# Kernel optimization log

Measured on AMD Instinct MI355X. Metric: run time of the kernel, lower is better.

The kernel has to match this reference:

```python
import jax, jax.numpy as jnp
import numpy as np

TAU = 2.0   # spikingjelly LIFNode default tau
VTH = 1.0   # config.vthreshold

@jax.custom_vjp
def atan_spike(x):
    # heaviside forward, ATan surrogate backward (spikingjelly surrogate.ATan, alpha=2)
    return (x >= 0).astype(x.dtype)

def _atan_fwd(x):
    return atan_spike(x), x

def _atan_bwd(x, g):
    alpha = 2.0
    return (g * (alpha / 2.0) / (1.0 + (jnp.pi / 2.0 * alpha * x) ** 2),)

atan_spike.defvjp(_atan_fwd, _atan_bwd)

def layer_norm(x, eps=1e-6):
    m = jnp.mean(x, axis=-1, keepdims=True)
    v = jnp.mean((x - m) ** 2, axis=-1, keepdims=True)
    return (x - m) * jax.lax.rsqrt(v + eps)

def time_shift(x):
    # ZeroPad2d((0,0,1,-1)): xx[:, t] = x[:, t-1], xx[:, 0] = 0
    return jnp.pad(x, ((0, 0), (1, 0), (0, 0)))[:, :-1]

def lif_multistep(x4):
    # spikingjelly LIFNode, step_mode='m', decay_input=True, hard reset to v_reset=0
    def step(v, xt):
        v = v + (xt - v) / TAU
        s = atan_spike(v - VTH)
        return v * (1.0 - s), s
    _, spikes = jax.lax.scan(step, jnp.zeros_like(x4[0]), x4)
    return spikes

def wkv(w, u, k, v):
    # RWKV-v4 numerically-stable WKV scan. w: [C] (negative), u: [C], k,v: [B,T,C]
    B, T, C = k.shape
    def step(carry, kv):
        aa, bb, pp = carry
        kt, vt = kv
        ww = u + kt
        p = jnp.maximum(pp, ww)
        e1 = jnp.exp(pp - p); e2 = jnp.exp(ww - p)
        y = (e1 * aa + e2 * vt) / (e1 * bb + e2)
        ww2 = pp + w
        p2 = jnp.maximum(ww2, kt)
        f1 = jnp.exp(ww2 - p2); f2 = jnp.exp(kt - p2)
        return (f1 * aa + f2 * vt, f1 * bb + f2, p2), y
    init = (jnp.zeros((B, C), k.dtype), jnp.zeros((B, C), k.dtype),
            jnp.full((B, C), -1e38, k.dtype))
    _, ys = jax.lax.scan(step, init, (jnp.moveaxis(k, 1, 0), jnp.moveaxis(v, 1, 0)))
    return jnp.moveaxis(ys, 0, 1)

def time_mix(h, time_decay, time_first, tmk, tmv, tmr, Wk, Wv, Wr, Wo):
    xx = time_shift(h)
    xk = h * tmk + xx * (1 - tmk)
    xv = h * tmv + xx * (1 - tmv)
    xr = h * tmr + xx * (1 - tmr)
    k = jnp.einsum('btc,oc->bto', xk, Wk)
    v = jnp.einsum('btc,oc->bto', xv, Wv)
    sr = jax.nn.sigmoid(jnp.einsum('btc,oc->bto', xr, Wr))
    y = wkv(-jnp.exp(time_decay), time_first, k, v)
    return jnp.einsum('btc,oc->bto', sr * y, Wo)

def channel_mix(h, cmk, cmr, Wck, Wcv, Wcr):
    xx = time_shift(h)
    xk = h * cmk + xx * (1 - cmk)
    xr = h * cmr + xx * (1 - cmr)
    k = jnp.square(jax.nn.relu(jnp.einsum('btc,hc->bth', xk, Wck)))
    kv = jnp.einsum('bth,ch->btc', k, Wcv)
    return jax.nn.sigmoid(jnp.einsum('btc,oc->bto', xr, Wcr)) * kv

def _forward(x, rt, time_decay, time_first, tmix_k, tmix_v, tmix_r,
             Wk, Wv, Wr, Wo, cmix_k, cmix_r, Wck, Wcv, Wcr,
             Wrm, brm, Wam, bam):
    B, P1, C = x.shape
    xc = jnp.concatenate([x, jnp.broadcast_to(rt, (B, P1, C))], axis=1)  # [B, 2*P1, C]
    att = time_mix(layer_norm(xc), time_decay, time_first,
                   tmix_k, tmix_v, tmix_r, Wk, Wv, Wr, Wo)
    att = lif_multistep(jnp.broadcast_to(att, (4,) + att.shape)).mean(0)
    xc = xc + att
    ffn = channel_mix(layer_norm(xc), cmix_k, cmix_r, Wck, Wcv, Wcr)
    ffn = lif_multistep(jnp.broadcast_to(ffn, (4,) + ffn.shape)).mean(0)
    xc = xc + ffn
    xo, rtok = xc[:, :P1], xc[:, P1:]
    r = jnp.einsum('bpc,qc->bpq', rtok, Wrm) + brm   # restruction_token_MLP [B,P1,P1]
    r = jnp.swapaxes(r, 1, 2)                        # permute(0,2,1)
    r = jnp.einsum('bpq,cq->bpc', r, Wam) + bam      # another_MLP [B,P1,C]
    return xo + xo * r

def setup_inputs() -> dict:
    key = jax.random.key(0)
    ks = jax.random.split(key, 20)
    B, P1, C = 8, 256, 1024
    H = 4 * C
    s = 0.02
    f32 = jnp.float32
    return {
        'x': jax.random.normal(ks[0], (B, P1, C), f32),
        'rt': jax.random.normal(ks[1], (1, P1, C), f32) * 0.5,
        'time_decay': jax.random.normal(ks[2], (C,), f32),
        'time_first': jax.random.normal(ks[3], (C,), f32) * 0.3,
        'tmix_k': jax.random.uniform(ks[4], (1, 1, C), f32),
        'tmix_v': jax.random.uniform(ks[5], (1, 1, C), f32),
        'tmix_r': jax.random.uniform(ks[6], (1, 1, C), f32),
        'Wk': jax.random.normal(ks[7], (C, C), f32) * s,
        'Wv': jax.random.normal(ks[8], (C, C), f32) * s,
        'Wr': jax.random.normal(ks[9], (C, C), f32) * s,
        'Wo': jax.random.normal(ks[10], (C, C), f32) * s,
        'cmix_k': jax.random.uniform(ks[11], (1, 1, C), f32),
        'cmix_r': jax.random.uniform(ks[12], (1, 1, C), f32),
        'Wck': jax.random.normal(ks[13], (H, C), f32) * s,
        'Wcv': jax.random.normal(ks[14], (C, H), f32) * s,
        'Wcr': jax.random.normal(ks[15], (C, C), f32) * s,
        'Wrm': jax.random.normal(ks[16], (P1, C), f32) * s,
        'brm': jax.random.normal(ks[17], (P1,), f32) * s,
        'Wam': jax.random.normal(ks[18], (C, P1), f32) * s,
        'bam': jax.random.normal(ks[19], (C,), f32) * s,
    }

def reference(x, rt, time_decay, time_first, tmix_k, tmix_v, tmix_r,
              Wk, Wv, Wr, Wo, cmix_k, cmix_r, Wck, Wcv, Wcr,
              Wrm, brm, Wam, bam):
    return _forward(x, rt, time_decay, time_first, tmix_k, tmix_v, tmix_r,
                    Wk, Wv, Wr, Wo, cmix_k, cmix_r, Wck, Wcv, Wcr,
                    Wrm, brm, Wam, bam)
```

## Files before the change

kernel.cpp:

```cpp
#include <hip/hip_runtime.h>
#include <hip/hip_bf16.h>
#include <math.h>
#include <stdint.h>

#define TB_ 8
#define TT_ 512
#define TC_ 1024
#define WKV_NCH 32
#define WKV_L 16

typedef __attribute__((ext_vector_type(8))) short bf16x8;
typedef __attribute__((ext_vector_type(4))) short s16x4;
typedef __attribute__((ext_vector_type(4))) float f32x4;

__device__ __forceinline__ float b2f(short u) {
  union { unsigned int i; float f; } x;
  x.i = ((unsigned int)(unsigned short)u) << 16;
  return x.f;
}
__device__ __forceinline__ short f2b(float f) {
  __hip_bfloat16 h = __float2bfloat16(f);
  return __builtin_bit_cast(short, h);
}
__device__ __forceinline__ float sigm(float x) { return 1.0f / (1.0f + expf(-x)); }

__device__ __forceinline__ float lif4(float a) {
  float v = 0.0f, acc = 0.0f;
#pragma unroll
  for (int i = 0; i < 4; ++i) {
    v += (a - v) * 0.5f;
    float s = (v >= 1.0f) ? 1.0f : 0.0f;
    acc += s;
    v *= (1.0f - s);
  }
  return acc * 0.25f;
}

__device__ __forceinline__ void gload16(const void* g, void* l) {
  __builtin_amdgcn_global_load_lds(
      (__attribute__((address_space(1))) void*)(g),
      (__attribute__((address_space(3))) void*)(l), 16, 0, 0);
}

template <int N>
__device__ __forceinline__ void waitv() {
  if constexpr (N == 0)  asm volatile("s_waitcnt vmcnt(0)" ::: "memory");
  else if constexpr (N == 2)  asm volatile("s_waitcnt vmcnt(2)" ::: "memory");
  else if constexpr (N == 4)  asm volatile("s_waitcnt vmcnt(4)" ::: "memory");
  else if constexpr (N == 8)  asm volatile("s_waitcnt vmcnt(8)" ::: "memory");
  else if constexpr (N == 12) asm volatile("s_waitcnt vmcnt(12)" ::: "memory");
  else static_assert(N == 0, "unsupported vmcnt");
}
__device__ __forceinline__ void barrier_() {
  asm volatile("s_barrier" ::: "memory");
}


__global__ __launch_bounds__(256) void ln_mix3(
    const float* __restrict__ x, const float* __restrict__ rt,
    const float* __restrict__ tmk, const float* __restrict__ tmv,
    const float* __restrict__ tmr, float* __restrict__ xc,
    short* __restrict__ xk, short* __restrict__ xv, short* __restrict__ xr) {
  __shared__ float red[256];
  int row = blockIdx.x;
  int t = row & 511, b = row >> 9;
  int tid = threadIdx.x;
  const float* src = (t < 256) ? x + (int64_t)(b * 256 + t) * TC_
                               : rt + (int64_t)(t - 256) * TC_;
  float4 v = ((const float4*)src)[tid];
  ((float4*)(xc + (int64_t)row * TC_))[tid] = v;
  red[tid] = v.x + v.y + v.z + v.w;
  __syncthreads();
  for (int off = 128; off > 0; off >>= 1) {
    if (tid < off) red[tid] += red[tid + off];
    __syncthreads();
  }
  float mean = red[0] * (1.0f / 1024.0f);
  __syncthreads();
  float dx = v.x - mean, dy = v.y - mean, dz = v.z - mean, dw = v.w - mean;
  red[tid] = dx * dx + dy * dy + dz * dz + dw * dw;
  __syncthreads();
  for (int off = 128; off > 0; off >>= 1) {
    if (tid < off) red[tid] += red[tid + off];
    __syncthreads();
  }
  float rs = 1.0f / sqrtf(red[0] * (1.0f / 1024.0f) + 1e-6f);
  float c0 = dx * rs, c1 = dy * rs, c2 = dz * rs, c3 = dw * rs;
  float p0 = 0.f, p1 = 0.f, p2 = 0.f, p3 = 0.f;
  if (t > 0) {
    int tp = t - 1;
    const float* srcp = (tp < 256) ? x + (int64_t)(b * 256 + tp) * TC_
                                   : rt + (int64_t)(tp - 256) * TC_;
    __syncthreads();
    float4 w4 = ((const float4*)srcp)[tid];
    red[tid] = w4.x + w4.y + w4.z + w4.w;
    __syncthreads();
    for (int off = 128; off > 0; off >>= 1) {
      if (tid < off) red[tid] += red[tid + off];
      __syncthreads();
    }
    float meanp = red[0] * (1.0f / 1024.0f);
    __syncthreads();
    float ex = w4.x - meanp, ey = w4.y - meanp, ez = w4.z - meanp,
          ew = w4.w - meanp;
    red[tid] = ex * ex + ey * ey + ez * ez + ew * ew;
    __syncthreads();
    for (int off = 128; off > 0; off >>= 1) {
      if (tid < off) red[tid] += red[tid + off];
      __syncthreads();
    }
    float rsp = 1.0f / sqrtf(red[0] * (1.0f / 1024.0f) + 1e-6f);
    p0 = ex * rsp; p1 = ey * rsp; p2 = ez * rsp; p3 = ew * rsp;
  }
  int c = tid * 4;
  int64_t o = (int64_t)row * TC_ + c;
  float m0, m1, m2, m3;
  s16x4 ov;
  m0 = tmk[c]; m1 = tmk[c + 1]; m2 = tmk[c + 2]; m3 = tmk[c + 3];
  ov.x = f2b(c0 * m0 + p0 * (1.0f - m0));
  ov.y = f2b(c1 * m1 + p1 * (1.0f - m1));
  ov.z = f2b(c2 * m2 + p2 * (1.0f - m2));
  ov.w = f2b(c3 * m3 + p3 * (1.0f - m3));
  *(s16x4*)(xk + o) = ov;
  m0 = tmv[c]; m1 = tmv[c + 1]; m2 = tmv[c + 2]; m3 = tmv[c + 3];
  ov.x = f2b(c0 * m0 + p0 * (1.0f - m0));
  ov.y = f2b(c1 * m1 + p1 * (1.0f - m1));
  ov.z = f2b(c2 * m2 + p2 * (1.0f - m2));
  ov.w = f2b(c3 * m3 + p3 * (1.0f - m3));
  *(s16x4*)(xv + o) = ov;
  m0 = tmr[c]; m1 = tmr[c + 1]; m2 = tmr[c + 2]; m3 = tmr[c + 3];
  ov.x = f2b(c0 * m0 + p0 * (1.0f - m0));
  ov.y = f2b(c1 * m1 + p1 * (1.0f - m1));
  ov.z = f2b(c2 * m2 + p2 * (1.0f - m2));
  ov.w = f2b(c3 * m3 + p3 * (1.0f - m3));
  *(s16x4*)(xr + o) = ov;
}

__global__ __launch_bounds__(256) void ln_mix2(const float* __restrict__ xc,
                                               const float* __restrict__ cmk,
                                               const float* __restrict__ cmr,
                                               short* __restrict__ xk,
                                               short* __restrict__ xr) {
  __shared__ float red[256];
  int row = blockIdx.x;
  int t = row & 511;
  int tid = threadIdx.x;
  float4 v = ((const float4*)(xc + (int64_t)row * TC_))[tid];
  red[tid] = v.x + v.y + v.z + v.w;
  __syncthreads();
  for (int off = 128; off > 0; off >>= 1) {
    if (tid < off) red[tid] += red[tid + off];
    __syncthreads();
  }
  float mean = red[0] * (1.0f / 1024.0f);
  __syncthreads();
  float dx = v.x - mean, dy = v.y - mean, dz = v.z - mean, dw = v.w - mean;
  red[tid] = dx * dx + dy * dy + dz * dz + dw * dw;
  __syncthreads();
  for (int off = 128; off > 0; off >>= 1) {
    if (tid < off) red[tid] += red[tid + off];
    __syncthreads();
  }
  float rs = 1.0f / sqrtf(red[0] * (1.0f / 1024.0f) + 1e-6f);
  float c0 = dx * rs, c1 = dy * rs, c2 = dz * rs, c3 = dw * rs;
  float p0 = 0.f, p1 = 0.f, p2 = 0.f, p3 = 0.f;
  if (t > 0) {
    __syncthreads();
    float4 w4 = ((const float4*)(xc + (int64_t)(row - 1) * TC_))[tid];
    red[tid] = w4.x + w4.y + w4.z + w4.w;
    __syncthreads();
    for (int off = 128; off > 0; off >>= 1) {
      if (tid < off) red[tid] += red[tid + off];
      __syncthreads();
    }
    float meanp = red[0] * (1.0f / 1024.0f);
    __syncthreads();
    float ex = w4.x - meanp, ey = w4.y - meanp, ez = w4.z - meanp,
          ew = w4.w - meanp;
    red[tid] = ex * ex + ey * ey + ez * ez + ew * ew;
    __syncthreads();
    for (int off = 128; off > 0; off >>= 1) {
      if (tid < off) red[tid] += red[tid + off];
      __syncthreads();
    }
    float rsp = 1.0f / sqrtf(red[0] * (1.0f / 1024.0f) + 1e-6f);
    p0 = ex * rsp; p1 = ey * rsp; p2 = ez * rsp; p3 = ew * rsp;
  }
  int c = tid * 4;
  float k0 = cmk[c], k1 = cmk[c + 1], k2 = cmk[c + 2], k3 = cmk[c + 3];
  float r0 = cmr[c], r1 = cmr[c + 1], r2 = cmr[c + 2], r3 = cmr[c + 3];
  s16x4 ok, orr;
  ok.x = f2b(c0 * k0 + p0 * (1.0f - k0));
  ok.y = f2b(c1 * k1 + p1 * (1.0f - k1));
  ok.z = f2b(c2 * k2 + p2 * (1.0f - k2));
  ok.w = f2b(c3 * k3 + p3 * (1.0f - k3));
  orr.x = f2b(c0 * r0 + p0 * (1.0f - r0));
  orr.y = f2b(c1 * r1 + p1 * (1.0f - r1));
  orr.z = f2b(c2 * r2 + p2 * (1.0f - r2));
  orr.w = f2b(c3 * r3 + p3 * (1.0f - r3));
  *(s16x4*)(xk + (int64_t)row * TC_ + c) = ok;
  *(s16x4*)(xr + (int64_t)row * TC_ + c) = orr;
}

__global__ __launch_bounds__(256) void cvt_b(const float* __restrict__ src,
                                             short* __restrict__ dst) {
  int64_t i = (int64_t)(blockIdx.x * 256 + threadIdx.x) * 8;
  float4 a = *(const float4*)(src + i);
  float4 b = *(const float4*)(src + i + 4);
  bf16x8 o;
  o[0] = f2b(a.x); o[1] = f2b(a.y); o[2] = f2b(a.z); o[3] = f2b(a.w);
  o[4] = f2b(b.x); o[5] = f2b(b.y); o[6] = f2b(b.z); o[7] = f2b(b.w);
  *(bf16x8*)(dst + i) = o;
}

__global__ __launch_bounds__(256) void cvt_rtok(const float* __restrict__ xc,
                                                short* __restrict__ dst) {
  int i = blockIdx.x * 256 + threadIdx.x;
  int b = i >> 15;
  int rem = i & 32767;
  const float* s = xc + (int64_t)b * 524288 + 262144 + (int64_t)rem * 8;
  float4 a = *(const float4*)s;
  float4 c = *(const float4*)(s + 4);
  bf16x8 o;
  o[0] = f2b(a.x); o[1] = f2b(a.y); o[2] = f2b(a.z); o[3] = f2b(a.w);
  o[4] = f2b(c.x); o[5] = f2b(c.y); o[6] = f2b(c.z); o[7] = f2b(c.w);
  *(bf16x8*)(dst + (int64_t)i * 8) = o;
}

__global__ __launch_bounds__(256) void cvt_all(
    const float* __restrict__ Wk, const float* __restrict__ Wv,
    const float* __restrict__ Wr, const float* __restrict__ Wo,
    const float* __restrict__ Wcr, const float* __restrict__ Wcv,
    const float* __restrict__ Wrm, const float* __restrict__ Wam,
    short* __restrict__ bWk, short* __restrict__ bWv, short* __restrict__ bWr,
    short* __restrict__ bWo, short* __restrict__ bWcr, short* __restrict__ bWcv,
    short* __restrict__ bWrm, short* __restrict__ bWam,
    float* __restrict__ S) {
  int bid = blockIdx.x;
  if (bid >= 4864) {
    int row = (bid - 4864) * 4 + (threadIdx.x >> 6);
    int lane = threadIdx.x & 63;
    float4 v = ((const float4*)(Wam + (int64_t)row * 256))[lane];
    float s = v.x + v.y + v.z + v.w;
    for (int off = 32; off > 0; off >>= 1) s += __shfl_down(s, off);
    if (lane == 0) S[row] = s;
    return;
  }
  const float* src; short* dst; int base;
  if (bid < 512)       { src = Wk;  dst = bWk;  base = bid; }
  else if (bid < 1024) { src = Wv;  dst = bWv;  base = bid - 512; }
  else if (bid < 1536) { src = Wr;  dst = bWr;  base = bid - 1024; }
  else if (bid < 2048) { src = Wo;  dst = bWo;  base = bid - 1536; }
  else if (bid < 2560) { src = Wcr; dst = bWcr; base = bid - 2048; }
  else if (bid < 4608) { src = Wcv; dst = bWcv; base = bid - 2560; }
  else if (bid < 4736) { src = Wrm; dst = bWrm; base = bid - 4608; }
  else                 { src = Wam; dst = bWam; base = bid - 4736; }
  int64_t i = ((int64_t)base * 256 + threadIdx.x) * 8;
  float4 a = *(const float4*)(src + i);
  float4 b = *(const float4*)(src + i + 4);
  bf16x8 o;
  o[0] = f2b(a.x); o[1] = f2b(a.y); o[2] = f2b(a.z); o[3] = f2b(a.w);
  o[4] = f2b(b.x); o[5] = f2b(b.y); o[6] = f2b(b.z); o[7] = f2b(b.w);
  *(bf16x8*)(dst + i) = o;
}

__global__ __launch_bounds__(256) void wkv_p1(const float* __restrict__ td,
                                              const short* __restrict__ K,
                                              const short* __restrict__ V,
                                              float* __restrict__ Ca,
                                              float* __restrict__ Da,
                                              float* __restrict__ Qa) {
  int bx = blockIdx.x;
  int ch = bx >> 5;
  int b = (bx >> 2) & 7;
  int c = (bx & 3) * 256 + threadIdx.x;
  float w = -expf(td[c]);
  float aa = 0.0f, bb = 0.0f, pp = -1e38f;
  int64_t base = ((int64_t)b * TT_ + ch * WKV_L) * TC_ + c;
#pragma unroll
  for (int t = 0; t < WKV_L; ++t) {
    int64_t o = base + (int64_t)t * TC_;
    float kt = b2f(K[o]), vt = b2f(V[o]);
    float ww2 = pp + w;
    float p2 = fmaxf(ww2, kt);
    float e1 = expf(ww2 - p2);
    float e2 = expf(kt - p2);
    aa = e1 * aa + e2 * vt;
    bb = e1 * bb + e2;
    pp = p2;
  }
  int idx = ch * 8192 + b * 1024 + c;
  Ca[idx] = aa; Da[idx] = bb; Qa[idx] = pp;
}

__global__ __launch_bounds__(256) void wkv_p2(const float* __restrict__ td,
                                              const float* __restrict__ Ca,
                                              const float* __restrict__ Da,
                                              const float* __restrict__ Qa,
                                              float* __restrict__ Aa,
                                              float* __restrict__ Ba,
                                              float* __restrict__ Pa) {
  int i = blockIdx.x * 256 + threadIdx.x;
  int c = i & (TC_ - 1);
  float wL = -expf(td[c]) * (float)WKV_L;
  float aa = 0.0f, bb = 0.0f, pp = -1e38f;
#pragma unroll 4
  for (int ch = 0; ch < WKV_NCH; ++ch) {
    int idx = ch * 8192 + i;
    Aa[idx] = aa; Ba[idx] = bb; Pa[idx] = pp;
    float ppw = pp + wL;
    float q = Qa[idx];
    float p2 = fmaxf(ppw, q);
    float ea = expf(ppw - p2);
    float eb = expf(q - p2);
    aa = aa * ea + Ca[idx] * eb;
    bb = bb * ea + Da[idx] * eb;
    pp = p2;
  }
}

__global__ __launch_bounds__(256) void wkv_p3(const float* __restrict__ td,
                                              const float* __restrict__ tf,
                                              const short* __restrict__ K,
                                              const short* __restrict__ V,
                                              const short* __restrict__ SR,
                                              short* __restrict__ SRY,
                                              const float* __restrict__ Aa,
                                              const float* __restrict__ Ba,
                                              const float* __restrict__ Pa) {
  int bx = blockIdx.x;
  int ch = bx >> 5;
  int b = (bx >> 2) & 7;
  int c = (bx & 3) * 256 + threadIdx.x;
  float w = -expf(td[c]);
  float u = tf[c];
  int idx = ch * 8192 + b * 1024 + c;
  float aa = Aa[idx], bb = Ba[idx], pp = Pa[idx];
  int64_t base = ((int64_t)b * TT_ + ch * WKV_L) * TC_ + c;
#pragma unroll
  for (int t = 0; t < WKV_L; ++t) {
    int64_t o = base + (int64_t)t * TC_;
    float kt = b2f(K[o]), vt = b2f(V[o]);
    float ww = u + kt;
    float p = fmaxf(pp, ww);
    float E1 = expf(pp - p);
    float E2 = expf(ww - p);
    float y = (E1 * aa + E2 * vt) / (E1 * bb + E2);
    SRY[o] = f2b(y * b2f(SR[o]));
    float ww2 = pp + w;
    float p2 = fmaxf(ww2, kt);
    float e1 = expf(ww2 - p2);
    float e2 = expf(kt - p2);
    aa = e1 * aa + e2 * vt;
    bb = e1 * bb + e2;
    pp = p2;
  }
}

template <int EPI>
__global__ __launch_bounds__(512, 1) void gemm4p(
    const short* __restrict__ A, const short* __restrict__ B,
    void* __restrict__ Cp, int M, int N, int K, int Kst,
    const float* __restrict__ e0, const float* __restrict__ e1,
    const float* __restrict__ e2, const void* __restrict__ e3) {
  __shared__ short lds[2 * 32768];
  const int tid = threadIdx.x;

  const unsigned gx = gridDim.x, gy = gridDim.y;
  const unsigned nwg = gx * gy;
  const unsigned lin = blockIdx.x + gx * blockIdx.y;
  const unsigned cs = nwg >> 3;
  const unsigned nl = (lin & 7) * cs + (lin >> 3);
  const unsigned bxs = nl % gx;
  const unsigned bys = nl / gx;

  const int brow = bys * 128;
  const int bcol = bxs * 128;

  const int srow = ((tid >> 6) << 4) + (tid & 15);
  const int skc = ((tid >> 4) & 3) * 8;
  const short* gA = A + (int64_t)(brow + srow) * Kst + skc;
  const short* gB = B + (int64_t)(bcol + srow) * Kst + skc;

  const int lane = tid & 63, wid = tid >> 6;
  const int wr = wid >> 2, wc = wid & 3;

  f32x4 acc[4][2] = {};

#define RD_A(rb, kh, m) \
  (*(const bf16x8*)(lds + (rb) * 32768 + (kh) * 8192 + (wr * 4 + (m)) * 512 + lane * 8))
#define RD_B(rb, kh, n) \
  (*(const bf16x8*)(lds + (rb) * 32768 + 16384 + (kh) * 8192 + (wc * 2 + (n)) * 512 + lane * 8))
#define ST_A(sb, kh, kt) \
  gload16(gA + (kt) * 64 + (kh) * 32, lds + (sb) * 32768 + (kh) * 8192 + tid * 8)
#define ST_B(sb, kh, kt) \
  gload16(gB + (kt) * 64 + (kh) * 32, lds + (sb) * 32768 + 16384 + (kh) * 8192 + tid * 8)
#define MM(am, bn, i, j) \
  acc[i][j] = __builtin_amdgcn_mfma_f32_16x16x32_bf16(am, bn, acc[i][j], 0, 0, 0)

  const int nt = K / 64;
  ST_A(0, 0, 0); ST_B(0, 0, 0); ST_A(0, 1, 0); ST_B(0, 1, 0);
  waitv<2>();
  barrier_();

  for (int t = 0; t < nt - 1; ++t) {
    const int rb = t & 1, sb = rb ^ 1, kn = t + 1;
    {
      bf16x8 a0 = RD_A(rb, 0, 0), a1 = RD_A(rb, 0, 1);
      bf16x8 b0 = RD_B(rb, 0, 0), b1 = RD_B(rb, 0, 1);
      ST_A(sb, 0, kn);
      MM(a0, b0, 0, 0); MM(a0, b1, 0, 1); MM(a1, b0, 1, 0); MM(a1, b1, 1, 1);
      barrier_();
      bf16x8 a2 = RD_A(rb, 0, 2), a3 = RD_A(rb, 0, 3);
      ST_B(sb, 0, kn);
      MM(a2, b0, 2, 0); MM(a2, b1, 2, 1); MM(a3, b0, 3, 0); MM(a3, b1, 3, 1);
      waitv<2>();
      barrier_();
    }
    {
      bf16x8 a0 = RD_A(rb, 1, 0), a1 = RD_A(rb, 1, 1);
      bf16x8 b0 = RD_B(rb, 1, 0), b1 = RD_B(rb, 1, 1);
      ST_A(sb, 1, kn);
      MM(a0, b0, 0, 0); MM(a0, b1, 0, 1); MM(a1, b0, 1, 0); MM(a1, b1, 1, 1);
      barrier_();
      bf16x8 a2 = RD_A(rb, 1, 2), a3 = RD_A(rb, 1, 3);
      ST_B(sb, 1, kn);
      MM(a2, b0, 2, 0); MM(a2, b1, 2, 1); MM(a3, b0, 3, 0); MM(a3, b1, 3, 1);
      waitv<2>();
      barrier_();
    }
  }
  {
    waitv<0>();
    barrier_();
    const int rb = (nt - 1) & 1;
#pragma unroll
    for (int kh = 0; kh < 2; ++kh) {
      bf16x8 a0 = RD_A(rb, kh, 0), a1 = RD_A(rb, kh, 1);
      bf16x8 a2 = RD_A(rb, kh, 2), a3 = RD_A(rb, kh, 3);
      bf16x8 b0 = RD_B(rb, kh, 0), b1 = RD_B(rb, kh, 1);
      MM(a0, b0, 0, 0); MM(a0, b1, 0, 1); MM(a1, b0, 1, 0); MM(a1, b1, 1, 1);
      MM(a2, b0, 2, 0); MM(a2, b1, 2, 1); MM(a3, b0, 3, 0); MM(a3, b1, 3, 1);
    }
  }
#undef RD_A
#undef RD_B
#undef ST_A
#undef ST_B
#undef MM

  const int r0 = brow + wr * 64 + (lane >> 4) * 4;
  const int c0 = bcol + wc * 32 + (lane & 15);
#pragma unroll
  for (int m = 0; m < 4; ++m) {
#pragma unroll
    for (int j = 0; j < 4; ++j) {
      int row = r0 + m * 16 + j;
#pragma unroll
      for (int n = 0; n < 2; ++n) {
        int col = c0 + n * 16;
        float v = acc[m][n][j];
        int64_t idx = (int64_t)row * N + col;
        if (EPI == 1) {
          ((short*)Cp)[idx] = f2b(sigm(v));
        } else if (EPI == 4) {
          float* XC = (float*)Cp;
          XC[idx] = XC[idx] + lif4(v);
        } else if (EPI == 5) {
          float* XC = (float*)Cp;
          float srr = b2f(((const short*)e3)[idx]);
          XC[idx] = XC[idx] + lif4(v * srr);
        }
      }
    }
  }
}

template <int BM, int BN, int EPI, int D, int MINW>
__global__ __launch_bounds__(256, MINW) void gemm_bf16(
    const short* __restrict__ A, const short* __restrict__ B,
    void* __restrict__ Cp, int M, int N, int K, int Kst,
    int64_t sA, int64_t sB, int64_t sC,
    const float* __restrict__ e0, const float* __restrict__ e1,
    const float* __restrict__ e2, const void* __restrict__ e3, int64_t sE) {
  constexpr int MF = BM / 32;
  constexpr int NF = BN / 32;
  constexpr int ASLOT = BM / 64;
  constexpr int BSLOT = BN / 64;
  constexpr int NL = ASLOT + BSLOT;
  constexpr int SBUF = (BM + BN) * 32;
  __shared__ short lds[D * SBUF];
  const int tid = threadIdx.x;

  const unsigned gx = gridDim.x, gy = gridDim.y;
  const unsigned nwg = gx * gy * gridDim.z;
  const unsigned lin = blockIdx.x + gx * (blockIdx.y + gy * blockIdx.z);
  const unsigned cs = nwg >> 3;
  const unsigned nl = (lin & 7) * cs + (lin >> 3);
  const unsigned bxs = nl % gx;
  const unsigned tmp = nl / gx;
  const unsigned bys = tmp % gy;
  const unsigned bz = tmp / gy;

  const int brow = bys * BM;
  const int bcol = bxs * BN;
  const short* Ab = A + bz * sA;
  const short* Bb = B + bz * sB;

  const int srow = ((tid >> 6) << 4) + (tid & 15);
  const int skc = ((tid >> 4) & 3) * 8;
  const short* gA[ASLOT];
  const short* gB[BSLOT];
#pragma unroll
  for (int s = 0; s < ASLOT; ++s)
    gA[s] = Ab + (int64_t)(brow + s * 64 + srow) * Kst + skc;
#pragma unroll
  for (int s = 0; s < BSLOT; ++s)
    gB[s] = Bb + (int64_t)(bcol + s * 64 + srow) * Kst + skc;

  const int lane = tid & 63, wid = tid >> 6;
  const int wr = wid >> 1, wc = wid & 1;

  f32x4 acc[MF][NF] = {};

  auto stage = [&](int buf, int k0) {
    short* d = lds + buf * SBUF;
#pragma unroll
    for (int s = 0; s < ASLOT; ++s)
      gload16(gA[s] + k0, d + s * 2048 + tid * 8);
#pragma unroll
    for (int s = 0; s < BSLOT; ++s)
      gload16(gB[s] + k0, d + BM * 32 + s * 2048 + tid * 8);
  };
  auto compute = [&](int buf) {
    const short* base = lds + buf * SBUF;
    bf16x8 af[MF], bfv[NF];
#pragma unroll
    for (int m = 0; m < MF; ++m)
      af[m] = *(const bf16x8*)(base + (wr * MF + m) * 512 + lane * 8);
#pragma unroll
    for (int n = 0; n < NF; ++n)
      bfv[n] = *(const bf16x8*)(base + BM * 32 + (wc * NF + n) * 512 + lane * 8);
#pragma unroll
    for (int m = 0; m < MF; ++m)
#pragma unroll
      for (int n = 0; n < NF; ++n)
        acc[m][n] = __builtin_amdgcn_mfma_f32_16x16x32_bf16(af[m], bfv[n],
                                                            acc[m][n], 0, 0, 0);
  };

  const int nst = K / 32;
#pragma unroll
  for (int d = 0; d < D - 1; ++d) stage(d, d * 32);
  for (int t = 0; t <= nst - D; ++t) {
    stage((t + D - 1) & (D - 1), (t + D - 1) * 32);
    waitv<(D - 1) * NL>();
    barrier_();
    compute(t & (D - 1));
    barrier_();
  }
  {
    int t = nst - D + 1;
    if constexpr (D >= 4) {
      waitv<2 * NL>(); barrier_(); compute(t & (D - 1)); barrier_(); ++t;
      waitv<1 * NL>(); barrier_(); compute(t & (D - 1)); barrier_(); ++t;
    }
    waitv<0>(); barrier_(); compute(t & (D - 1));
  }

  const int r0 = brow + wr * (BM / 2) + (lane >> 4) * 4;
  const int c0 = bcol + wc * (BN / 2) + (lane & 15);
#pragma unroll
  for (int m = 0; m < MF; ++m) {
#pragma unroll
    for (int j = 0; j < 4; ++j) {
      int row = r0 + m * 16 + j;
#pragma unroll
      for (int n = 0; n < NF; ++n) {
        int col = c0 + n * 16;
        float v = acc[m][n][j];
        int64_t idx = (int64_t)row * N + col;
        if (EPI == 0) {
          ((short*)Cp)[bz * sC + idx] = f2b(v);
        } else if (EPI == 2) {
          v = fmaxf(v, 0.0f);
          ((short*)Cp)[bz * sC + idx] = f2b(v * v);
        } else if (EPI == 3) {
          float r2 = v + e0[row] * e1[col] + e2[col];
          float xo = ((const float*)e3)[bz * sE + idx];
          ((float*)Cp)[bz * sC + idx] = xo * (1.0f + r2);
        } else if (EPI == 6) {
          ((short*)Cp)[bz * sC + idx] = f2b(bz == 2 ? sigm(v) : v);
        }
      }
    }
  }
}

extern "C" void kernel_launch(void* const* d_in, const int* in_sizes, int n_in,
                              void* d_out, int out_size, void* d_ws,
                              size_t ws_size, hipStream_t stream) {
  const float* x   = (const float*)d_in[0];
  const float* rt  = (const float*)d_in[1];
  const float* td  = (const float*)d_in[2];
  const float* tf  = (const float*)d_in[3];
  const float* tmk = (const float*)d_in[4];
  const float* tmv = (const float*)d_in[5];
  const float* tmr = (const float*)d_in[6];
  const float* Wk  = (const float*)d_in[7];
  const float* Wv  = (const float*)d_in[8];
  const float* Wr  = (const float*)d_in[9];
  const float* Wo  = (const float*)d_in[10];
  const float* cmk = (const float*)d_in[11];
  const float* cmr = (const float*)d_in[12];
  const float* Wck = (const float*)d_in[13];
  const float* Wcv = (const float*)d_in[14];
  const float* Wcr = (const float*)d_in[15];
  const float* Wrm = (const float*)d_in[16];
  const float* brm = (const float*)d_in[17];
  const float* Wam = (const float*)d_in[18];
  const float* bam = (const float*)d_in[19];
  float* out = (float*)d_out;

  const size_t MB = 1ull << 20;
  uint8_t* W8 = (uint8_t*)d_ws;
  float* XC   = (float*)(W8);
  short* S1   = (short*)(W8 + 24 * MB);
  short* S2   = (short*)(W8 + 32 * MB);
  short* S3   = (short*)(W8 + 40 * MB);
  short* bWcv = (short*)(W8 + 48 * MB);
  short* bWk  = (short*)(W8 + 56 * MB);
  short* bWo  = (short*)(W8 + 62 * MB);
  short* bWcr = (short*)(W8 + 64 * MB);
  short* bWrm = (short*)(W8 + 66 * MB);
  short* bWam = (short*)(W8 + 66 * MB + 512 * 1024);
  short* KK   = (short*)(W8 + 67 * MB);
  short* VV   = (short*)(W8 + 75 * MB);
  short* RR   = (short*)(W8 + 83 * MB);
  float* Ca   = (float*)(W8 + 91 * MB);
  float* Da   = (float*)(W8 + 92 * MB);
  float* Qa   = (float*)(W8 + 93 * MB);
  float* Aa   = (float*)(W8 + 94 * MB);
  float* Ba   = (float*)(W8 + 95 * MB);
  float* Pa   = (float*)(W8 + 96 * MB);
  short* SRY  = S1;
  short* xk2  = S2;
  short* xr2  = S3;
  short* SRR  = S1;
  short* bWck = S3;
  short* H16  = KK;
  short* rtok = S2;
  short* Mt   = (short*)(W8 + 36 * MB);
  float* Sb   = (float*)(W8 + 99 * MB);

  dim3 blk(256);
  dim3 blk512(512);

  cvt_all<<<5120, blk, 0, stream>>>(Wk, Wv, Wr, Wo, Wcr, Wcv, Wrm, Wam,
                                    bWk, bWk + 1048576, bWk + 2097152, bWo,
                                    bWcr, bWcv, bWrm, bWam, Sb);

  ln_mix3<<<TB_ * TT_, blk, 0, stream>>>(x, rt, tmk, tmv, tmr, XC, S1, S2, S3);

  gemm_bf16<128, 128, 6, 2, 3><<<dim3(8, 32, 3), blk, 0, stream>>>(
      S1, bWk, KK, 4096, 1024, 1024, 1024, 4194304, 1048576, 4194304,
      nullptr, nullptr, nullptr, nullptr, 0);
  wkv_p1<<<WKV_NCH * TB_ * 4, blk, 0, stream>>>(td, KK, VV, Ca, Da, Qa);
  wkv_p2<<<32, blk, 0, stream>>>(td, Ca, Da, Qa, Aa, Ba, Pa);
  wkv_p3<<<WKV_NCH * TB_ * 4, blk, 0, stream>>>(td, tf, KK, VV, RR, SRY,
                                                Aa, Ba, Pa);
  gemm4p<4><<<dim3(8, 32), blk512, 0, stream>>>(
      SRY, bWo, XC, 4096, 1024, 1024, 1024, nullptr, nullptr, nullptr,
      nullptr);
  ln_mix2<<<TB_ * TT_, blk, 0, stream>>>(XC, cmk, cmr, xk2, xr2);
  gemm4p<1><<<dim3(8, 32), blk512, 0, stream>>>(
      xr2, bWcr, SRR, 4096, 1024, 1024, 1024, nullptr, nullptr, nullptr,
      nullptr);
  cvt_b<<<2048, blk, 0, stream>>>(Wck, bWck);
  gemm_bf16<128, 128, 2, 2, 4><<<dim3(32, 32, 1), blk, 0, stream>>>(
      xk2, bWck, H16, 4096, 4096, 1024, 1024, 0, 0, 0,
      nullptr, nullptr, nullptr, nullptr, 0);
  gemm4p<5><<<dim3(8, 32), blk512, 0, stream>>>(
      H16, bWcv, XC, 4096, 1024, 4096, 4096, nullptr, nullptr, nullptr, SRR);
  cvt_rtok<<<1024, blk, 0, stream>>>(XC, rtok);
  gemm_bf16<64, 64, 0, 2, 2><<<dim3(4, 4, 8), blk, 0, stream>>>(
      bWrm, rtok, Mt, 256, 256, 1024, 1024, 0, (int64_t)256 * 1024,
      (int64_t)256 * 256, nullptr, nullptr, nullptr, nullptr, 0);
  gemm_bf16<64, 64, 3, 2, 2><<<dim3(16, 4, 8), blk, 0, stream>>>(
      Mt, bWam, out, 256, 1024, 256, 256, (int64_t)256 * 256, 0,
      (int64_t)256 * 1024, brm, Sb, bam, XC, (int64_t)512 * 1024);
}
```

Before: 328.6 us.

## Add 256x256-tile 512-thread GEMM with interleaved loads for channel-mix key projection

Adds a new gemm256 kernel that uses 256x256 output tiles, 8 waves, and double-buffered LDS, with global-to-LDS loads for the next k-tile interleaved between MFMA groups. It replaces the 128x128 gemm_bf16 call for the 4096x4096x1024 squared-ReLU key projection in channel mix. The larger tile raises arithmetic intensity and cuts global traffic, at the cost of one workgroup per CU (256 workgroups) and heavy register pressure from 32 accumulators per thread.

```diff
diff --git a/kernel.cpp b/kernel.cpp
--- a/kernel.cpp
+++ b/kernel.cpp
@@ -476,6 +476,160 @@
   }
 }
 
+template <int EPI>
+__global__ __launch_bounds__(512, 1) void gemm256(
+    const short* __restrict__ A, const short* __restrict__ B,
+    void* __restrict__ Cp, int M, int N, int K, int Kst) {
+  __shared__ short lds[2 * 32768];
+  const int tid = threadIdx.x;
+
+  const unsigned gx = gridDim.x, gy = gridDim.y;
+  const unsigned nwg = gx * gy;
+  const unsigned lin = blockIdx.x + gx * blockIdx.y;
+  const unsigned cs = nwg >> 3;
+  const unsigned nl = (lin & 7) * cs + (lin >> 3);
+  const unsigned bxs = nl % gx;
+  const unsigned bys = nl / gx;
+
+  const int brow = bys * 256;
+  const int bcol = bxs * 256;
+
+  const short* gA[2];
+  const short* gB[2];
+  int loff[2];
+#pragma unroll
+  for (int c = 0; c < 2; ++c) {
+    int p = c * 512 + tid;
+    int u = p >> 6, s = p & 63;
+    gA[c] = A + (int64_t)(brow + u * 16 + (s & 15)) * Kst + (s >> 4) * 8;
+    gB[c] = B + (int64_t)(bcol + u * 16 + (s & 15)) * Kst + (s >> 4) * 8;
+    loff[c] = p * 8;
+  }
+
+  const int lane = tid & 63, wid = tid >> 6;
+  const int wr = wid >> 2, wc = wid & 3;
+
+  f32x4 acc[8][4] = {};
+
+#define RD_A(rb, kh, m) \
+  (*(const bf16x8*)(lds + (rb) * 32768 + (kh) * 8192 + (wr * 8 + (m)) * 512 + lane * 8))
+#define RD_B(rb, kh, n) \
+  (*(const bf16x8*)(lds + (rb) * 32768 + 16384 + (kh) * 8192 + (wc * 4 + (n)) * 512 + lane * 8))
+#define ST_A(sb, kh, kt)                                                     \
+  {                                                                          \
+    gload16(gA[0] + (kt) * 64 + (kh) * 32,                                   \
+            lds + (sb) * 32768 + (kh) * 8192 + loff[0]);                     \
+    gload16(gA[1] + (kt) * 64 + (kh) * 32,                                   \
+            lds + (sb) * 32768 + (kh) * 8192 + loff[1]);                     \
+  }
+#define ST_B(sb, kh, kt)                                                     \
+  {                                                                          \
+    gload16(gB[0] + (kt) * 64 + (kh) * 32,                                   \
+            lds + (sb) * 32768 + 16384 + (kh) * 8192 + loff[0]);             \
+    gload16(gB[1] + (kt) * 64 + (kh) * 32,                                   \
+            lds + (sb) * 32768 + 16384 + (kh) * 8192 + loff[1]);             \
+  }
+#define MM(am, bn, i, j) \
+  acc[i][j] = __builtin_amdgcn_mfma_f32_16x16x32_bf16(am, bn, acc[i][j], 0, 0, 0)
+
+  const int nt = K / 64;
+  ST_A(0, 0, 0); ST_B(0, 0, 0); ST_A(0, 1, 0); ST_B(0, 1, 0);
+  waitv<4>();
+  barrier_();
+
+  for (int t = 0; t < nt - 1; ++t) {
+    const int rb = t & 1, sb = rb ^ 1, kn = t + 1;
+    bf16x8 b0, b1, b2, b3;
+    {
+      bf16x8 a0 = RD_A(rb, 0, 0), a1 = RD_A(rb, 0, 1);
+      bf16x8 a2 = RD_A(rb, 0, 2), a3 = RD_A(rb, 0, 3);
+      b0 = RD_B(rb, 0, 0); b1 = RD_B(rb, 0, 1);
+      b2 = RD_B(rb, 0, 2); b3 = RD_B(rb, 0, 3);
+      ST_A(sb, 0, kn);
+      MM(a0, b0, 0, 0); MM(a0, b1, 0, 1); MM(a0, b2, 0, 2); MM(a0, b3, 0, 3);
+      MM(a1, b0, 1, 0); MM(a1, b1, 1, 1); MM(a1, b2, 1, 2); MM(a1, b3, 1, 3);
+      MM(a2, b0, 2, 0); MM(a2, b1, 2, 1); MM(a2, b2, 2, 2); MM(a2, b3, 2, 3);
+      MM(a3, b0, 3, 0); MM(a3, b1, 3, 1); MM(a3, b2, 3, 2); MM(a3, b3, 3, 3);
+      barrier_();
+    }
+    {
+      bf16x8 a4 = RD_A(rb, 0, 4), a5 = RD_A(rb, 0, 5);
+      bf16x8 a6 = RD_A(rb, 0, 6), a7 = RD_A(rb, 0, 7);
+      ST_B(sb, 0, kn);
+      MM(a4, b0, 4, 0); MM(a4, b1, 4, 1); MM(a4, b2, 4, 2); MM(a4, b3, 4, 3);
+      MM(a5, b0, 5, 0); MM(a5, b1, 5, 1); MM(a5, b2, 5, 2); MM(a5, b3, 5, 3);
+      MM(a6, b0, 6, 0); MM(a6, b1, 6, 1); MM(a6, b2, 6, 2); MM(a6, b3, 6, 3);
+      MM(a7, b0, 7, 0); MM(a7, b1, 7, 1); MM(a7, b2, 7, 2); MM(a7, b3, 7, 3);
+      waitv<4>();
+      barrier_();
+    }
+    {
+      bf16x8 a0 = RD_A(rb, 1, 0), a1 = RD_A(rb, 1, 1);
+      bf16x8 a2 = RD_A(rb, 1, 2), a3 = RD_A(rb, 1, 3);
+      b0 = RD_B(rb, 1, 0); b1 = RD_B(rb, 1, 1);
+      b2 = RD_B(rb, 1, 2); b3 = RD_B(rb, 1, 3);
+      ST_A(sb, 1, kn);
+      MM(a0, b0, 0, 0); MM(a0, b1, 0, 1); MM(a0, b2, 0, 2); MM(a0, b3, 0, 3);
+      MM(a1, b0, 1, 0); MM(a1, b1, 1, 1); MM(a1, b2, 1, 2); MM(a1, b3, 1, 3);
+      MM(a2, b0, 2, 0); MM(a2, b1, 2, 1); MM(a2, b2, 2, 2); MM(a2, b3, 2, 3);
+      MM(a3, b0, 3, 0); MM(a3, b1, 3, 1); MM(a3, b2, 3, 2); MM(a3, b3, 3, 3);
+      barrier_();
+    }
+    {
+      bf16x8 a4 = RD_A(rb, 1, 4), a5 = RD_A(rb, 1, 5);
+      bf16x8 a6 = RD_A(rb, 1, 6), a7 = RD_A(rb, 1, 7);
+      ST_B(sb, 1, kn);
+      MM(a4, b0, 4, 0); MM(a4, b1, 4, 1); MM(a4, b2, 4, 2); MM(a4, b3, 4, 3);
+      MM(a5, b0, 5, 0); MM(a5, b1, 5, 1); MM(a5, b2, 5, 2); MM(a5, b3, 5, 3);
+      MM(a6, b0, 6, 0); MM(a6, b1, 6, 1); MM(a6, b2, 6, 2); MM(a6, b3, 6, 3);
+      MM(a7, b0, 7, 0); MM(a7, b1, 7, 1); MM(a7, b2, 7, 2); MM(a7, b3, 7, 3);
+      waitv<4>();
+      barrier_();
+    }
+  }
+  {
+    waitv<0>();
+    barrier_();
+    const int rb = (nt - 1) & 1;
+#pragma unroll
+    for (int kh = 0; kh < 2; ++kh) {
+      bf16x8 b0 = RD_B(rb, kh, 0), b1 = RD_B(rb, kh, 1);
+      bf16x8 b2 = RD_B(rb, kh, 2), b3 = RD_B(rb, kh, 3);
+#pragma unroll
+      for (int m = 0; m < 8; ++m) {
+        bf16x8 am = RD_A(rb, kh, m);
+        MM(am, b0, m, 0); MM(am, b1, m, 1);
+        MM(am, b2, m, 2); MM(am, b3, m, 3);
+      }
+    }
+  }
+#undef RD_A
+#undef RD_B
+#undef ST_A
+#undef ST_B
+#undef MM
+
+  const int r0 = brow + wr * 128 + (lane >> 4) * 4;
+  const int c0 = bcol + wc * 64 + (lane & 15);
+#pragma unroll
+  for (int m = 0; m < 8; ++m) {
+#pragma unroll
+    for (int j = 0; j < 4; ++j) {
+      int row = r0 + m * 16 + j;
+#pragma unroll
+      for (int n = 0; n < 4; ++n) {
+        int col = c0 + n * 16;
+        float v = acc[m][n][j];
+        int64_t idx = (int64_t)row * N + col;
+        if (EPI == 2) {
+          v = fmaxf(v, 0.0f);
+          ((short*)Cp)[idx] = f2b(v * v);
+        }
+      }
+    }
+  }
+}
+
 template <int BM, int BN, int EPI, int D, int MINW>
 __global__ __launch_bounds__(256, MINW) void gemm_bf16(
     const short* __restrict__ A, const short* __restrict__ B,
@@ -582,9 +736,6 @@
         int64_t idx = (int64_t)row * N + col;
         if (EPI == 0) {
           ((short*)Cp)[bz * sC + idx] = f2b(v);
-        } else if (EPI == 2) {
-          v = fmaxf(v, 0.0f);
-          ((short*)Cp)[bz * sC + idx] = f2b(v * v);
         } else if (EPI == 3) {
           float r2 = v + e0[row] * e1[col] + e2[col];
           float xo = ((const float*)e3)[bz * sE + idx];
@@ -677,9 +828,8 @@
       xr2, bWcr, SRR, 4096, 1024, 1024, 1024, nullptr, nullptr, nullptr,
       nullptr);
   cvt_b<<<2048, blk, 0, stream>>>(Wck, bWck);
-  gemm_bf16<128, 128, 2, 2, 4><<<dim3(32, 32, 1), blk, 0, stream>>>(
-      xk2, bWck, H16, 4096, 4096, 1024, 1024, 0, 0, 0,
-      nullptr, nullptr, nullptr, nullptr, 0);
+  gemm256<2><<<dim3(16, 16), blk512, 0, stream>>>(
+      xk2, bWck, H16, 4096, 4096, 1024, 1024);
   gemm4p<5><<<dim3(8, 32), blk512, 0, stream>>>(
       H16, bWcv, XC, 4096, 1024, 4096, 4096, nullptr, nullptr, nullptr, SRR);
   cvt_rtok<<<1024, blk, 0, stream>>>(XC, rtok);
```

After: 304.6 us. 7.3% less time.
